# Kernel optimization log

Hardware: AMD Instinct MI355X
Metric: run time of the kernel (lower is better)

Reference implementation:

```python
import jax, jax.numpy as jnp
import numpy as np

D_MODEL = 2048
N_Q_HEADS = 32
N_KV_HEADS = 8
HEAD_DIM = D_MODEL // N_Q_HEADS  # 64
KV_DIM = HEAD_DIM * N_KV_HEADS   # 512
B, S = 2, 2048


def setup_inputs() -> dict:
    key = jax.random.key(0)
    ks = jax.random.split(key, 11)
    sc_d = 1.0 / np.sqrt(D_MODEL)
    return {
        "query": jax.random.normal(ks[0], (B, S, D_MODEL), jnp.float32),
        "key":   jax.random.normal(ks[1], (B, S, D_MODEL), jnp.float32),
        "value": jax.random.normal(ks[2], (B, S, D_MODEL), jnp.float32),
        "Wq": jax.random.normal(ks[3], (D_MODEL, D_MODEL), jnp.float32) * sc_d,
        "bq": jnp.zeros((D_MODEL,), jnp.float32),
        "Wk": jax.random.normal(ks[4], (D_MODEL, KV_DIM), jnp.float32) * sc_d,
        "bk": jnp.zeros((KV_DIM,), jnp.float32),
        "Wv": jax.random.normal(ks[5], (D_MODEL, KV_DIM), jnp.float32) * sc_d,
        "bv": jnp.zeros((KV_DIM,), jnp.float32),
        "Wo": jax.random.normal(ks[6], (D_MODEL, D_MODEL), jnp.float32) * sc_d,
        "bo": jnp.zeros((D_MODEL,), jnp.float32),
    }


def reference(query, key, value, Wq, bq, Wk, bk, Wv, bv, Wo, bo):
    b, s, _ = query.shape
    g = N_Q_HEADS // N_KV_HEADS  # num groups
    # projections
    Q = query @ Wq + bq                      # [b, s, d_model]
    K = key @ Wk + bk                        # [b, s, kv_dim]
    V = value @ Wv + bv                      # [b, s, kv_dim]
    # split heads. Torch code splits Q into groups of num_kv_heads heads,
    # and each group broadcasts per-head against the Hkv KV heads, i.e.
    # query head (grp*Hkv + j) attends against kv head j.
    Q = Q.reshape(b, s, g, N_KV_HEADS, HEAD_DIM)  # [b, s, g, hkv, d]
    K = K.reshape(b, s, N_KV_HEADS, HEAD_DIM)     # [b, s, hkv, d]
    V = V.reshape(b, s, N_KV_HEADS, HEAD_DIM)
    scale = 1.0 / jnp.sqrt(jnp.float32(HEAD_DIM))
    scores = jnp.einsum('bsghd,bthd->bghst', Q, K) * scale  # [b,g,hkv,s,s]
    attn = jax.nn.softmax(scores, axis=-1)
    out = jnp.einsum('bghst,bthd->bsghd', attn, V)          # [b,s,g,hkv,d]
    # concat over groups then heads == original head order (g major, hkv minor)
    out = out.reshape(b, s, D_MODEL)
    return out @ Wo + bo
```

## Files before the change

kernel.cpp:

```cpp
#include <hip/hip_runtime.h>
#include <cstdint>

typedef _Float16 half4 __attribute__((ext_vector_type(4)));
typedef _Float16 half8 __attribute__((ext_vector_type(8)));
typedef _Float16 half16 __attribute__((ext_vector_type(16)));
typedef float f32x4 __attribute__((ext_vector_type(4)));
typedef float f32x16 __attribute__((ext_vector_type(16)));

#define L2E 1.44269504088896340736f

__device__ __forceinline__ void gl16(const void* g, void* l) {
  __builtin_amdgcn_global_load_lds(
      (const __attribute__((address_space(1))) void*)g,
      (__attribute__((address_space(3))) void*)l, 16, 0, 0);
}

__device__ __forceinline__ uint32_t pk2(float a, float b) {
  return __builtin_bit_cast(uint32_t, __builtin_amdgcn_cvt_pkrtz(a, b));
}

__device__ __forceinline__ void plswap(uint32_t& x, uint32_t& y) {
  auto r = __builtin_amdgcn_permlane32_swap((int)x, (int)y, false, false);
  x = (uint32_t)r[0];
  y = (uint32_t)r[1];
}

__device__ __forceinline__ f32x16 zero16() {
  f32x16 z;
  #pragma unroll
  for (int r = 0; r < 16; ++r) z[r] = 0.0f;
  return z;
}

__global__ __launch_bounds__(256) void prep_all(
    const float* __restrict__ q, const float* __restrict__ k, const float* __restrict__ v,
    const float* __restrict__ Wq, const float* __restrict__ Wk,
    const float* __restrict__ Wv, const float* __restrict__ Wo,
    _Float16* __restrict__ qh, _Float16* __restrict__ kh, _Float16* __restrict__ vh,
    _Float16* __restrict__ WqkvT, _Float16* __restrict__ WoT)
{
  int id = blockIdx.x;
  const int tid = threadIdx.y * 32 + threadIdx.x;
  if (id < 12288) {
    const int z = id >> 12;
    const int x = id & 4095;
    const float* src = (z == 0) ? q : (z == 1 ? k : v);
    _Float16* dst    = (z == 0) ? qh : (z == 1 ? kh : vh);
    size_t i = ((size_t)x * 256 + tid) * 8;
    float4 a = *(const float4*)(src + i);
    float4 b = *(const float4*)(src + i + 4);
    half8 o;
    o[0] = (_Float16)a.x; o[1] = (_Float16)a.y; o[2] = (_Float16)a.z; o[3] = (_Float16)a.w;
    o[4] = (_Float16)b.x; o[5] = (_Float16)b.y; o[6] = (_Float16)b.z; o[7] = (_Float16)b.w;
    *(half8*)(dst + i) = o;
    return;
  }
  id -= 12288;
  const float* src;
  _Float16* dst;
  int N, tx, ty;
  if (id < 4096)      { src = Wq; dst = WqkvT;                        N = 2048; tx = id & 63; ty = id >> 6; }
  else if (id < 5120) { id -= 4096; src = Wk; dst = WqkvT + (size_t)2048 * 2048; N = 512; tx = id & 15; ty = id >> 4; }
  else if (id < 6144) { id -= 5120; src = Wv; dst = WqkvT + (size_t)2560 * 2048; N = 512; tx = id & 15; ty = id >> 4; }
  else                { id -= 6144; src = Wo; dst = WoT;              N = 2048; tx = id & 63; ty = id >> 6; }
  const int n0 = tx * 32, k0 = ty * 32;
  __shared__ float t[32][33];
  #pragma unroll
  for (int i = 0; i < 4; ++i)
    t[threadIdx.y + i * 8][threadIdx.x] =
        src[(size_t)(k0 + threadIdx.y + i * 8) * N + n0 + threadIdx.x];
  __syncthreads();
  #pragma unroll
  for (int i = 0; i < 4; ++i)
    dst[(size_t)(n0 + threadIdx.y + i * 8) * 2048 + k0 + threadIdx.x] =
        (_Float16)t[threadIdx.x][threadIdx.y + i * 8];
}

template<int MODE>
__global__ __launch_bounds__(512, 2) void gemm128(
    const _Float16* __restrict__ Aq, const _Float16* __restrict__ Ak, const _Float16* __restrict__ Av,
    const _Float16* __restrict__ Bt,
    const float* __restrict__ bias0, const float* __restrict__ bias1, const float* __restrict__ bias2,
    _Float16* __restrict__ Ch, float* __restrict__ Cf, _Float16* __restrict__ VTo)
{
  constexpr int K = 2048;
  constexpr int N = (MODE == 0) ? 3072 : 2048;
  constexpr int NB = N / 128;
  constexpr int G = 32 * NB;
  constexpr int BUF = 8192 + 8192;
  constexpr int TPAD = 136;

  const int wg = blockIdx.x;
  const int work = (wg & 7) * (G / 8) + (wg >> 3);
  const int m0 = (work / NB) * 128;
  const int n0 = (work % NB) * 128;

  const _Float16* A = Aq;
  if constexpr (MODE == 0) { if (n0 >= 2560) A = Av; else if (n0 >= 2048) A = Ak; }

  const int tid = threadIdx.x;
  const int lane = tid & 63;
  const int w = tid >> 6;
  const int wr = w >> 2;
  const int wc = w & 3;
  const int lo = lane & 15, hi = lane >> 4;

  __shared__ __align__(1024) char smem[3 * BUF];

  f32x4 acc[4][2];
  #pragma unroll
  for (int mt = 0; mt < 4; ++mt)
    #pragma unroll
    for (int nt = 0; nt < 2; ++nt)
      acc[mt][nt] = (f32x4){0.f, 0.f, 0.f, 0.f};

  const _Float16* pB = Bt + (size_t)(n0 + w * 16 + (lane >> 2)) * K + (lane & 3) * 8;
  const _Float16* pA = A  + (size_t)(m0 + w * 16 + (lane >> 2)) * K + (lane & 3) * 8;
  const int dstB = 8192 + w * 1024;
  const int dstA = w * 1024;

  #define STAGE(base)                                                         \
    do {                                                                      \
      gl16(pA, (base) + dstA);                                                \
      gl16(pB, (base) + dstB);                                                \
    } while (0)

  STAGE(smem);
  pA += 32; pB += 32;
  STAGE(smem + BUF);
  pA += 32; pB += 32;
  asm volatile("s_waitcnt vmcnt(2)" ::: "memory");
  __builtin_amdgcn_s_barrier();

  const int abase = (wr * 64 + lo) * 64 + hi * 16;
  const int bbase = 8192 + (wc * 32 + lo) * 64 + hi * 16;

  int c = 0;
  for (int t = 0; t < 64; ++t) {
    int c1 = c + 1; if (c1 == 3) c1 = 0;
    int c2 = c1 + 1; if (c2 == 3) c2 = 0;
    if (t < 62) {
      STAGE(smem + c2 * BUF);
      pA += 32; pB += 32;
    }

    const char* bc = smem + c * BUF;
    half8 af[4], bf[2];
    #pragma unroll
    for (int mt = 0; mt < 4; ++mt) af[mt] = *(const half8*)(bc + abase + mt * 1024);
    #pragma unroll
    for (int nt = 0; nt < 2; ++nt) bf[nt] = *(const half8*)(bc + bbase + nt * 1024);

    __builtin_amdgcn_s_setprio(1);
    #pragma unroll
    for (int mt = 0; mt < 4; ++mt)
      #pragma unroll
      for (int nt = 0; nt < 2; ++nt)
        acc[mt][nt] = __builtin_amdgcn_mfma_f32_16x16x32_f16(af[mt], bf[nt], acc[mt][nt], 0, 0, 0);
    __builtin_amdgcn_s_setprio(0);

    if (t < 62)       asm volatile("s_waitcnt vmcnt(2)" ::: "memory");
    else if (t == 62) asm volatile("s_waitcnt vmcnt(0)" ::: "memory");
    if (t < 63) __builtin_amdgcn_s_barrier();
    c = c1;
  }
  #undef STAGE

  const bool isV = (MODE == 0) && (n0 >= 2560);
  float* T = (float*)smem;
  const int tr = tid >> 4;
  const int sc = tid & 15;
  #pragma unroll
  for (int mp = 0; mp < 4; ++mp) {
    __syncthreads();
    #pragma unroll
    for (int nt = 0; nt < 2; ++nt)
      #pragma unroll
      for (int r = 0; r < 4; ++r)
        T[(wr * 16 + 4 * hi + r) * TPAD + wc * 32 + nt * 16 + lo] = acc[mp][nt][r];
    __syncthreads();
    if (isV) {
      const int cv = tid & 127;
      const int tg = tid >> 7;
      const int run = tg >> 1, hb = tg & 1;
      const int vd = n0 - 2560 + cv;
      const int hV = vd >> 6, dV = vd & 63;
      const float bias = bias2[vd];
      const int trow0 = run * 16 + hb * 8;
      const int tglob = m0 + run * 64 + mp * 16 + hb * 8;
      const int bb = tglob >> 11;
      const int tloc = tglob & 2047;
      half8 o;
      #pragma unroll
      for (int e = 0; e < 8; ++e)
        o[e] = (_Float16)(T[(trow0 + e) * TPAD + cv] + bias);
      *(half8*)(VTo + ((size_t)(bb * 8 + hV) * 64 + dV) * 2048 + tloc) = o;
    } else {
      const int grow = m0 + (tr >> 4) * 64 + mp * 16 + (tr & 15);
      const int gcol = n0 + sc * 8;
      const float* Trow = T + tr * TPAD + sc * 8;
      const float* bp = bias0;
      int cb = gcol;
      if constexpr (MODE == 0) {
        if (gcol >= 2048) { bp = bias1; cb = gcol - 2048; }
      }
      float4 v0 = ((const float4*)Trow)[0];
      float4 v1 = ((const float4*)Trow)[1];
      float4 b0 = ((const float4*)(bp + cb))[0];
      float4 b1 = ((const float4*)(bp + cb))[1];
      if constexpr (MODE == 0) {
        half8 o;
        o[0] = (_Float16)(v0.x + b0.x); o[1] = (_Float16)(v0.y + b0.y);
        o[2] = (_Float16)(v0.z + b0.z); o[3] = (_Float16)(v0.w + b0.w);
        o[4] = (_Float16)(v1.x + b1.x); o[5] = (_Float16)(v1.y + b1.y);
        o[6] = (_Float16)(v1.z + b1.z); o[7] = (_Float16)(v1.w + b1.w);
        *(half8*)(Ch + (size_t)grow * N + gcol) = o;
      } else {
        float* dstp = Cf + (size_t)grow * N + gcol;
        float4 o0 = {v0.x + b0.x, v0.y + b0.y, v0.z + b0.z, v0.w + b0.w};
        float4 o1 = {v1.x + b1.x, v1.y + b1.y, v1.z + b1.z, v1.w + b1.w};
        ((float4*)dstp)[0] = o0;
        ((float4*)dstp)[1] = o1;
      }
    }
  }
}

__global__ __launch_bounds__(256, 4) void attn_fwd4(
    const _Float16* __restrict__ QKV, const _Float16* __restrict__ VT,
    _Float16* __restrict__ AO)
{
  const int wg = blockIdx.x;
  const int work = (wg & 7) * 128 + (wg >> 3);
  const int bh = work >> 6;
  const int b = bh >> 3, h = bh & 7;
  const int rem = work & 63;
  const int qh = (rem >> 4) * 8 + h;
  const int qt = rem & 15;

  const int tid = threadIdx.x;
  const int lane = tid & 63;
  const int w = tid >> 6;
  const int l31 = lane & 31;
  const int hi5 = lane >> 5;
  const int r7 = l31 & 7;

  __shared__ __align__(1024) char sm[2][2][8192];

  const _Float16 QSC = (_Float16)(0.125f * L2E);
  const int qrow0 = b * 2048 + qt * 128 + w * 32 + l31;
  half8 qf[4];
  {
    const _Float16* qp = QKV + (size_t)qrow0 * 3072 + qh * 64 + hi5 * 8;
    #pragma unroll
    for (int s = 0; s < 4; ++s) {
      half8 q = *(const half8*)(qp + s * 16);
      #pragma unroll
      for (int e = 0; e < 8; ++e) q[e] = q[e] * QSC;
      qf[s] = q;
    }
  }

  const int li = lane >> 3;
  const int lc = lane & 7;
  const int kslot = lc ^ li;
  const int w16li = w * 16 + li;
  const _Float16* Ksrc = QKV + ((size_t)(b * 2048 + w16li)) * 3072 + 2048 + h * 64 + kslot * 8;
  const _Float16* Vsrc = VT + ((size_t)(b * 8 + h) * 64 + w16li) * 2048 + kslot * 8;

  f32x16 oa[2];
  oa[0] = zero16();
  oa[1] = zero16();
  float lreg = 0.f;

  {
    char* kd = &sm[0][0][0] + w * 2048;
    char* vd = &sm[0][1][0] + w * 2048;
    gl16(Ksrc, kd);
    gl16(Ksrc + (size_t)8 * 3072, kd + 1024);
    gl16(Vsrc, vd);
    gl16(Vsrc + (size_t)8 * 2048, vd + 1024);
  }
  __syncthreads();

  int cur = 0;
  for (int t = 0; t < 32; ++t) {
    if (t < 31) {
      const int t0 = (t + 1) * 64;
      char* kd = &sm[cur ^ 1][0][0] + w * 2048;
      char* vd = &sm[cur ^ 1][1][0] + w * 2048;
      const _Float16* kg = Ksrc + (size_t)t0 * 3072;
      const _Float16* vg = Vsrc + t0;
      gl16(kg, kd);
      gl16(kg + (size_t)8 * 3072, kd + 1024);
      gl16(vg, vd);
      gl16(vg + (size_t)8 * 2048, vd + 1024);
    }

    const char* Kb = &sm[cur][0][0];
    const char* Vb = &sm[cur][1][0];

    uint32_t pw[4][4];
    float ps = 0.f;
    #pragma unroll
    for (int j = 0; j < 2; ++j) {
      f32x16 sa = zero16();
      const int kr = j * 32 + l31;
      __builtin_amdgcn_s_setprio(1);
      #pragma unroll
      for (int s = 0; s < 4; ++s) {
        half8 kf = *(const half8*)(Kb + kr * 128 + (((2 * s + hi5) ^ r7) << 4));
        sa = __builtin_amdgcn_mfma_f32_32x32x16_f16(kf, qf[s], sa, 0, 0, 0);
      }
      __builtin_amdgcn_s_setprio(0);
      #pragma unroll
      for (int r = 0; r < 16; ++r) {
        const float p = __builtin_amdgcn_exp2f(sa[r]);
        sa[r] = p;
        ps += p;
      }
      #pragma unroll
      for (int hf = 0; hf < 2; ++hf) {
        const int rb = hf * 8;
        uint32_t w0 = pk2(sa[rb + 0], sa[rb + 1]);
        uint32_t w1 = pk2(sa[rb + 2], sa[rb + 3]);
        uint32_t w2 = pk2(sa[rb + 4], sa[rb + 5]);
        uint32_t w3 = pk2(sa[rb + 6], sa[rb + 7]);
        plswap(w0, w2);
        plswap(w1, w3);
        const int s = 2 * j + hf;
        pw[s][0] = w0; pw[s][1] = w1; pw[s][2] = w2; pw[s][3] = w3;
      }
    }
    ps += __shfl_xor(ps, 32);
    lreg += ps;

    __builtin_amdgcn_s_setprio(1);
    #pragma unroll
    for (int s = 0; s < 4; ++s) {
      union { uint32_t u[4]; half8 h; } p0;
      #pragma unroll
      for (int u = 0; u < 4; ++u) p0.u[u] = pw[s][u];
      #pragma unroll
      for (int i = 0; i < 2; ++i) {
        const int vr = i * 32 + l31;
        half8 vf = *(const half8*)(Vb + vr * 128 + (((2 * s + hi5) ^ r7) << 4));
        oa[i] = __builtin_amdgcn_mfma_f32_32x32x16_f16(vf, p0.h, oa[i], 0, 0, 0);
      }
    }
    __builtin_amdgcn_s_setprio(0);

    __syncthreads();
    cur ^= 1;
  }

  {
    const float inv = 1.0f / lreg;
    #pragma unroll
    for (int i = 0; i < 2; ++i) {
      _Float16* dst = AO + (size_t)qrow0 * 2048 + qh * 64 + i * 32 + hi5 * 4;
      #pragma unroll
      for (int q = 0; q < 4; ++q) {
        union { uint32_t u[2]; half4 h4; } o;
        o.u[0] = pk2(oa[i][4 * q + 0] * inv, oa[i][4 * q + 1] * inv);
        o.u[1] = pk2(oa[i][4 * q + 2] * inv, oa[i][4 * q + 3] * inv);
        *(half4*)(dst + 8 * q) = o.h4;
      }
    }
  }
}

extern "C" void kernel_launch(void* const* d_in, const int* in_sizes, int n_in,
                              void* d_out, int out_size, void* d_ws, size_t ws_size,
                              hipStream_t stream) {
  const float* query = (const float*)d_in[0];
  const float* key   = (const float*)d_in[1];
  const float* value = (const float*)d_in[2];
  const float* Wq = (const float*)d_in[3];
  const float* bq = (const float*)d_in[4];
  const float* Wk = (const float*)d_in[5];
  const float* bk = (const float*)d_in[6];
  const float* Wv = (const float*)d_in[7];
  const float* bv = (const float*)d_in[8];
  const float* Wo = (const float*)d_in[9];
  const float* bo = (const float*)d_in[10];
  float* out = (float*)d_out;

  char* ws = (char*)d_ws;
  _Float16* qh    = (_Float16*)(ws);
  _Float16* kh    = (_Float16*)(ws + 16777216);
  _Float16* vh    = (_Float16*)(ws + 33554432);
  _Float16* WqkvT = (_Float16*)(ws + 50331648);
  _Float16* WoT   = (_Float16*)(ws + 62914560);
  _Float16* QKVh  = (_Float16*)(ws + 71303168);
  _Float16* VT    = (_Float16*)(ws + 96468992);
  _Float16* aoh   = (_Float16*)(ws + 100663296);

  prep_all<<<22528, dim3(32, 8), 0, stream>>>(query, key, value, Wq, Wk, Wv, Wo,
                                              qh, kh, vh, WqkvT, WoT);
  gemm128<0><<<768, 512, 0, stream>>>(qh, kh, vh, WqkvT, bq, bk, bv,
                                      QKVh, nullptr, VT);
  attn_fwd4<<<1024, 256, 0, stream>>>(QKVh, VT, aoh);
  gemm128<1><<<512, 512, 0, stream>>>(aoh, nullptr, nullptr, WoT, bo,
                                      nullptr, nullptr, nullptr, out, nullptr);
}
```

Baseline: 231.8 us.

## Process two query heads per attention block to reuse K/V tiles

```diff
diff --git a/kernel.cpp b/kernel.cpp
--- a/kernel.cpp
+++ b/kernel.cpp
@@ -226,17 +226,18 @@
   }
 }
 
-__global__ __launch_bounds__(256, 4) void attn_fwd4(
+__global__ __launch_bounds__(256, 2) void attn_fwd6(
     const _Float16* __restrict__ QKV, const _Float16* __restrict__ VT,
     _Float16* __restrict__ AO)
 {
   const int wg = blockIdx.x;
-  const int work = (wg & 7) * 128 + (wg >> 3);
-  const int bh = work >> 6;
+  const int work = (wg & 7) * 64 + (wg >> 3);
+  const int bh = work >> 5;
   const int b = bh >> 3, h = bh & 7;
-  const int rem = work & 63;
-  const int qh = (rem >> 4) * 8 + h;
+  const int rem = work & 31;
+  const int qp = rem >> 4;
   const int qt = rem & 15;
+  const int qh0 = (2 * qp) * 8 + h;
 
   const int tid = threadIdx.x;
   const int lane = tid & 63;
@@ -249,15 +250,16 @@
 
   const _Float16 QSC = (_Float16)(0.125f * L2E);
   const int qrow0 = b * 2048 + qt * 128 + w * 32 + l31;
-  half8 qf[4];
-  {
-    const _Float16* qp = QKV + (size_t)qrow0 * 3072 + qh * 64 + hi5 * 8;
+  half8 qf[2][4];
+  #pragma unroll
+  for (int g = 0; g < 2; ++g) {
+    const _Float16* qp_ = QKV + (size_t)qrow0 * 3072 + (qh0 + g * 8) * 64 + hi5 * 8;
     #pragma unroll
     for (int s = 0; s < 4; ++s) {
-      half8 q = *(const half8*)(qp + s * 16);
+      half8 q = *(const half8*)(qp_ + s * 16);
       #pragma unroll
       for (int e = 0; e < 8; ++e) q[e] = q[e] * QSC;
-      qf[s] = q;
+      qf[g][s] = q;
     }
   }
 
@@ -268,10 +270,13 @@
   const _Float16* Ksrc = QKV + ((size_t)(b * 2048 + w16li)) * 3072 + 2048 + h * 64 + kslot * 8;
   const _Float16* Vsrc = VT + ((size_t)(b * 8 + h) * 64 + w16li) * 2048 + kslot * 8;
 
-  f32x16 oa[2];
-  oa[0] = zero16();
-  oa[1] = zero16();
-  float lreg = 0.f;
+  f32x16 oa[2][2];
+  #pragma unroll
+  for (int g = 0; g < 2; ++g) {
+    oa[g][0] = zero16();
+    oa[g][1] = zero16();
+  }
+  float lreg[2] = {0.f, 0.f};
 
   {
     char* kd = &sm[0][0][0] + w * 2048;
@@ -300,52 +305,62 @@
     const char* Kb = &sm[cur][0][0];
     const char* Vb = &sm[cur][1][0];
 
-    uint32_t pw[4][4];
-    float ps = 0.f;
+    uint32_t pw[2][4][4];
+    float ps0 = 0.f, ps1 = 0.f;
     #pragma unroll
     for (int j = 0; j < 2; ++j) {
-      f32x16 sa = zero16();
       const int kr = j * 32 + l31;
-      __builtin_amdgcn_s_setprio(1);
-      #pragma unroll
-      for (int s = 0; s < 4; ++s) {
-        half8 kf = *(const half8*)(Kb + kr * 128 + (((2 * s + hi5) ^ r7) << 4));
-        sa = __builtin_amdgcn_mfma_f32_32x32x16_f16(kf, qf[s], sa, 0, 0, 0);
+      half8 kf[4];
+      #pragma unroll
+      for (int s = 0; s < 4; ++s)
+        kf[s] = *(const half8*)(Kb + kr * 128 + (((2 * s + hi5) ^ r7) << 4));
+      #pragma unroll
+      for (int g = 0; g < 2; ++g) {
+        f32x16 sa = zero16();
+        __builtin_amdgcn_s_setprio(1);
+        #pragma unroll
+        for (int s = 0; s < 4; ++s)
+          sa = __builtin_amdgcn_mfma_f32_32x32x16_f16(kf[s], qf[g][s], sa, 0, 0, 0);
+        __builtin_amdgcn_s_setprio(0);
+        float psl = 0.f;
+        #pragma unroll
+        for (int r = 0; r < 16; ++r) {
+          const float p = __builtin_amdgcn_exp2f(sa[r]);
+          sa[r] = p;
+          psl += p;
+        }
+        if (g == 0) ps0 += psl; else ps1 += psl;
+        #pragma unroll
+        for (int hf = 0; hf < 2; ++hf) {
+          const int rb = hf * 8;
+          uint32_t w0 = pk2(sa[rb + 0], sa[rb + 1]);
+          uint32_t w1 = pk2(sa[rb + 2], sa[rb + 3]);
+          uint32_t w2 = pk2(sa[rb + 4], sa[rb + 5]);
+          uint32_t w3 = pk2(sa[rb + 6], sa[rb + 7]);
+          plswap(w0, w2);
+          plswap(w1, w3);
+          const int s = 2 * j + hf;
+          pw[g][s][0] = w0; pw[g][s][1] = w1; pw[g][s][2] = w2; pw[g][s][3] = w3;
+        }
       }
-      __builtin_amdgcn_s_setprio(0);
-      #pragma unroll
-      for (int r = 0; r < 16; ++r) {
-        const float p = __builtin_amdgcn_exp2f(sa[r]);
-        sa[r] = p;
-        ps += p;
-      }
-      #pragma unroll
-      for (int hf = 0; hf < 2; ++hf) {
-        const int rb = hf * 8;
-        uint32_t w0 = pk2(sa[rb + 0], sa[rb + 1]);
-        uint32_t w1 = pk2(sa[rb + 2], sa[rb + 3]);
-        uint32_t w2 = pk2(sa[rb + 4], sa[rb + 5]);
-        uint32_t w3 = pk2(sa[rb + 6], sa[rb + 7]);
-        plswap(w0, w2);
-        plswap(w1, w3);
-        const int s = 2 * j + hf;
-        pw[s][0] = w0; pw[s][1] = w1; pw[s][2] = w2; pw[s][3] = w3;
-      }
-    }
-    ps += __shfl_xor(ps, 32);
-    lreg += ps;
+    }
+    ps0 += __shfl_xor(ps0, 32);
+    ps1 += __shfl_xor(ps1, 32);
+    lreg[0] += ps0;
+    lreg[1] += ps1;
 
     __builtin_amdgcn_s_setprio(1);
     #pragma unroll
     for (int s = 0; s < 4; ++s) {
-      union { uint32_t u[4]; half8 h; } p0;
-      #pragma unroll
-      for (int u = 0; u < 4; ++u) p0.u[u] = pw[s][u];
+      union { uint32_t u[4]; half8 h; } p0, p1;
+      #pragma unroll
+      for (int u = 0; u < 4; ++u) { p0.u[u] = pw[0][s][u]; p1.u[u] = pw[1][s][u]; }
       #pragma unroll
       for (int i = 0; i < 2; ++i) {
         const int vr = i * 32 + l31;
         half8 vf = *(const half8*)(Vb + vr * 128 + (((2 * s + hi5) ^ r7) << 4));
-        oa[i] = __builtin_amdgcn_mfma_f32_32x32x16_f16(vf, p0.h, oa[i], 0, 0, 0);
+        oa[0][i] = __builtin_amdgcn_mfma_f32_32x32x16_f16(vf, p0.h, oa[0][i], 0, 0, 0);
+        oa[1][i] = __builtin_amdgcn_mfma_f32_32x32x16_f16(vf, p1.h, oa[1][i], 0, 0, 0);
       }
     }
     __builtin_amdgcn_s_setprio(0);
@@ -354,16 +369,17 @@
     cur ^= 1;
   }
 
-  {
-    const float inv = 1.0f / lreg;
+  #pragma unroll
+  for (int g = 0; g < 2; ++g) {
+    const float inv = 1.0f / lreg[g];
     #pragma unroll
     for (int i = 0; i < 2; ++i) {
-      _Float16* dst = AO + (size_t)qrow0 * 2048 + qh * 64 + i * 32 + hi5 * 4;
+      _Float16* dst = AO + (size_t)qrow0 * 2048 + (qh0 + g * 8) * 64 + i * 32 + hi5 * 4;
       #pragma unroll
       for (int q = 0; q < 4; ++q) {
         union { uint32_t u[2]; half4 h4; } o;
-        o.u[0] = pk2(oa[i][4 * q + 0] * inv, oa[i][4 * q + 1] * inv);
-        o.u[1] = pk2(oa[i][4 * q + 2] * inv, oa[i][4 * q + 3] * inv);
+        o.u[0] = pk2(oa[g][i][4 * q + 0] * inv, oa[g][i][4 * q + 1] * inv);
+        o.u[1] = pk2(oa[g][i][4 * q + 2] * inv, oa[g][i][4 * q + 3] * inv);
         *(half4*)(dst + 8 * q) = o.h4;
       }
     }
@@ -400,7 +416,7 @@
                                               qh, kh, vh, WqkvT, WoT);
   gemm128<0><<<768, 512, 0, stream>>>(qh, kh, vh, WqkvT, bq, bk, bv,
                                       QKVh, nullptr, VT);
-  attn_fwd4<<<1024, 256, 0, stream>>>(QKVh, VT, aoh);
+  attn_fwd6<<<512, 256, 0, stream>>>(QKVh, VT, aoh);
   gemm128<1><<<512, 512, 0, stream>>>(aoh, nullptr, nullptr, WoT, bo,
                                       nullptr, nullptr, nullptr, out, nullptr);
 }
```

New measurement: 238.8 us. 3.0% more time.

## Load K tiles directly into registers instead of staging through LDS

Applied to the files above, without the earlier changes.

```diff
diff --git a/kernel.cpp b/kernel.cpp
--- a/kernel.cpp
+++ b/kernel.cpp
@@ -226,7 +226,7 @@
   }
 }
 
-__global__ __launch_bounds__(256, 4) void attn_fwd4(
+__global__ __launch_bounds__(256, 4) void attn_fwd7(
     const _Float16* __restrict__ QKV, const _Float16* __restrict__ VT,
     _Float16* __restrict__ AO)
 {
@@ -245,7 +245,7 @@
   const int hi5 = lane >> 5;
   const int r7 = l31 & 7;
 
-  __shared__ __align__(1024) char sm[2][2][8192];
+  __shared__ __align__(1024) char sm[2][8192];
 
   const _Float16 QSC = (_Float16)(0.125f * L2E);
   const int qrow0 = b * 2048 + qt * 128 + w * 32 + l31;
@@ -265,53 +265,48 @@
   const int lc = lane & 7;
   const int kslot = lc ^ li;
   const int w16li = w * 16 + li;
-  const _Float16* Ksrc = QKV + ((size_t)(b * 2048 + w16li)) * 3072 + 2048 + h * 64 + kslot * 8;
   const _Float16* Vsrc = VT + ((size_t)(b * 8 + h) * 64 + w16li) * 2048 + kslot * 8;
+
+  const _Float16* Kth = QKV + ((size_t)(b * 2048 + l31)) * 3072 + 2048 + h * 64 + hi5 * 8;
 
   f32x16 oa[2];
   oa[0] = zero16();
   oa[1] = zero16();
   float lreg = 0.f;
 
+  half8 kreg[8];
   {
-    char* kd = &sm[0][0][0] + w * 2048;
-    char* vd = &sm[0][1][0] + w * 2048;
-    gl16(Ksrc, kd);
-    gl16(Ksrc + (size_t)8 * 3072, kd + 1024);
+    char* vd = &sm[0][0] + w * 2048;
     gl16(Vsrc, vd);
     gl16(Vsrc + (size_t)8 * 2048, vd + 1024);
+    #pragma unroll
+    for (int j = 0; j < 2; ++j)
+      #pragma unroll
+      for (int s = 0; s < 4; ++s)
+        kreg[4 * j + s] = *(const half8*)(Kth + (size_t)j * 32 * 3072 + s * 16);
   }
   __syncthreads();
 
   int cur = 0;
   for (int t = 0; t < 32; ++t) {
     if (t < 31) {
-      const int t0 = (t + 1) * 64;
-      char* kd = &sm[cur ^ 1][0][0] + w * 2048;
-      char* vd = &sm[cur ^ 1][1][0] + w * 2048;
-      const _Float16* kg = Ksrc + (size_t)t0 * 3072;
-      const _Float16* vg = Vsrc + t0;
-      gl16(kg, kd);
-      gl16(kg + (size_t)8 * 3072, kd + 1024);
+      char* vd = &sm[cur ^ 1][0] + w * 2048;
+      const _Float16* vg = Vsrc + (t + 1) * 64;
       gl16(vg, vd);
       gl16(vg + (size_t)8 * 2048, vd + 1024);
     }
 
-    const char* Kb = &sm[cur][0][0];
-    const char* Vb = &sm[cur][1][0];
+    const char* Vb = &sm[cur][0];
 
     uint32_t pw[4][4];
     float ps = 0.f;
     #pragma unroll
     for (int j = 0; j < 2; ++j) {
       f32x16 sa = zero16();
-      const int kr = j * 32 + l31;
       __builtin_amdgcn_s_setprio(1);
       #pragma unroll
-      for (int s = 0; s < 4; ++s) {
-        half8 kf = *(const half8*)(Kb + kr * 128 + (((2 * s + hi5) ^ r7) << 4));
-        sa = __builtin_amdgcn_mfma_f32_32x32x16_f16(kf, qf[s], sa, 0, 0, 0);
-      }
+      for (int s = 0; s < 4; ++s)
+        sa = __builtin_amdgcn_mfma_f32_32x32x16_f16(kreg[4 * j + s], qf[s], sa, 0, 0, 0);
       __builtin_amdgcn_s_setprio(0);
       #pragma unroll
       for (int r = 0; r < 16; ++r) {
@@ -332,6 +327,16 @@
         pw[s][0] = w0; pw[s][1] = w1; pw[s][2] = w2; pw[s][3] = w3;
       }
     }
+
+    if (t < 31) {
+      const _Float16* kg = Kth + (size_t)(t + 1) * 64 * 3072;
+      #pragma unroll
+      for (int j = 0; j < 2; ++j)
+        #pragma unroll
+        for (int s = 0; s < 4; ++s)
+          kreg[4 * j + s] = *(const half8*)(kg + (size_t)j * 32 * 3072 + s * 16);
+    }
+
     ps += __shfl_xor(ps, 32);
     lreg += ps;
 
@@ -400,7 +405,7 @@
                                               qh, kh, vh, WqkvT, WoT);
   gemm128<0><<<768, 512, 0, stream>>>(qh, kh, vh, WqkvT, bq, bk, bv,
                                       QKVh, nullptr, VT);
-  attn_fwd4<<<1024, 256, 0, stream>>>(QKVh, VT, aoh);
+  attn_fwd7<<<1024, 256, 0, stream>>>(QKVh, VT, aoh);
   gemm128<1><<<512, 512, 0, stream>>>(aoh, nullptr, nullptr, WoT, bo,
                                       nullptr, nullptr, nullptr, out, nullptr);
 }
```

Measured after the change: 281.4 us. 21.4% more time.
